# Kernel optimization log

Measured on AMD Instinct MI355X. Metric: run time of the kernel, lower is better.

The kernel has to match this reference:

```python
import jax, jax.numpy as jnp
import numpy as np

N_NODES = 50000
N_EDGES = 800000
N_LABEL_EDGES = 200000
IN_CH = 256
HID = 64
OUT_CH = 64


def gcn_conv(x, W, b, edge_index, n_nodes):
    """PyG GCNConv: symmetric-normalized aggregation with self-loops.
    out[col] = sum_row norm(row,col) * (x @ W)[row] + b
    """
    xw = x @ W  # [N, out]
    loops = jnp.arange(n_nodes, dtype=edge_index.dtype)
    row = jnp.concatenate([edge_index[0], loops])  # source
    col = jnp.concatenate([edge_index[1], loops])  # target
    deg = jax.ops.segment_sum(jnp.ones_like(col, dtype=xw.dtype), col, num_segments=n_nodes)
    dis = jnp.where(deg > 0, jax.lax.rsqrt(deg), 0.0)
    norm = dis[row] * dis[col]  # [E+N]
    out = jax.ops.segment_sum(xw[row] * norm[:, None], col, num_segments=n_nodes)
    return out + b


def setup_inputs() -> dict:
    key = jax.random.key(0)
    k0, k1, k2, k3, k4 = jax.random.split(key, 5)
    x = jax.random.normal(k0, (N_NODES, IN_CH), dtype=jnp.float32)
    edge_index = jax.random.randint(k1, (2, N_EDGES), 0, N_NODES, dtype=jnp.int32)
    edge_label_index = jax.random.randint(k2, (2, N_LABEL_EDGES), 0, N_NODES, dtype=jnp.int32)
    W1 = jax.random.normal(k3, (IN_CH, HID), dtype=jnp.float32) * (1.0 / np.sqrt(IN_CH))
    b1 = jnp.zeros((HID,), dtype=jnp.float32)
    W2 = jax.random.normal(k4, (HID, OUT_CH), dtype=jnp.float32) * (1.0 / np.sqrt(HID))
    b2 = jnp.zeros((OUT_CH,), dtype=jnp.float32)
    return {"x": x, "edge_index": edge_index, "edge_label_index": edge_label_index,
            "W1": W1, "b1": b1, "W2": W2, "b2": b2}


def reference(x, edge_index, edge_label_index, W1, b1, W2, b2):
    n = x.shape[0]
    # encode: two GCNConv layers with ReLU between
    h = jax.nn.relu(gcn_conv(x, W1, b1, edge_index, n))
    z = gcn_conv(h, W2, b2, edge_index, n)
    # decode: gather node pairs, elementwise multiply, sum over features
    src, dst = edge_label_index[0], edge_label_index[1]
    return jnp.sum(z[src] * z[dst], axis=1)  # [N_LABEL_EDGES]
```

## Files before the change

kernel.cpp:

```cpp
#include <hip/hip_runtime.h>
#include <hip/hip_bf16.h>


constexpr int NC = 512;
constexpr int NBPAD = 256;
constexpr int BSHIFT = 8;

using short8 = __attribute__((ext_vector_type(8))) short;
using f32x4 = __attribute__((ext_vector_type(4))) float;

__device__ __forceinline__ unsigned short f2bf(float f) {
    unsigned u = __float_as_uint(f);
    return (unsigned short)((u + 0x7FFF + ((u >> 16) & 1)) >> 16);
}
__device__ __forceinline__ float bf2f(unsigned short h) {
    return __uint_as_float(((unsigned)h) << 16);
}

__global__ __launch_bounds__(256) void pack_kernel(const float* __restrict__ W1,
                                                   const float* __restrict__ W2,
                                                   unsigned short* __restrict__ Wp1,
                                                   unsigned short* __restrict__ Wp2,
                                                   int* __restrict__ bsums) {
    const int t = threadIdx.x, b = blockIdx.x;
    if (b == 0) {
        bsums[t] = 0;
    } else if (b <= 64) {
        const int idx = (b - 1) * 256 + t;
        const int k = idx >> 6, c = idx & 63;
        Wp1[((k >> 3) * 64 + c) * 8 + (k & 7)] = f2bf(W1[idx]);
    } else {
        const int idx = (b - 65) * 256 + t;
        const int k = idx >> 6, c = idx & 63;
        Wp2[((k >> 3) * 64 + c) * 8 + (k & 7)] = f2bf(W2[idx]);
    }
}

__global__ __launch_bounds__(256) void hist_kernel(const int* __restrict__ col,
                                                   int* __restrict__ histBM,
                                                   int* __restrict__ bsums, int E, int CE) {
    __shared__ int hl[NBPAD];
    const int t = threadIdx.x, c = blockIdx.x;
    hl[t] = 0;
    __syncthreads();
    const int s = c * CE, e = min(E, s + CE);
    for (int i = s + t; i < e; i += 256) atomicAdd(&hl[col[i] >> BSHIFT], 1);
    __syncthreads();
    const int v = hl[t];
    histBM[t * NC + c] = v;
    if (v) atomicAdd(&bsums[t], v);
}

__global__ __launch_bounds__(256) void rowscan_kernel(const int* __restrict__ histBM,
                                                      const int* __restrict__ bsums,
                                                      int* __restrict__ offsBM) {
    __shared__ int red[256];
    __shared__ int sc[256];
    const int t = threadIdx.x, b = blockIdx.x;
    red[t] = (t < b) ? bsums[t] : 0;
    __syncthreads();
    for (int off = 128; off > 0; off >>= 1) {
        if (t < off) red[t] += red[t + off];
        __syncthreads();
    }
    const int base = red[0];
    const int2 a = *(const int2*)&histBM[b * NC + 2 * t];
    const int a0 = a.x, a1 = a.y;
    const int ps = a0 + a1;
    sc[t] = ps;
    __syncthreads();
    for (int off = 1; off < 256; off <<= 1) {
        int u = (t >= off) ? sc[t - off] : 0;
        __syncthreads();
        sc[t] += u;
        __syncthreads();
    }
    const int excl = sc[t] - ps;
    offsBM[b * NC + 2 * t] = base + excl;
    offsBM[b * NC + 2 * t + 1] = base + excl + a0;
}

__global__ __launch_bounds__(256) void reorder_kernel(const int* __restrict__ row,
                                                      const int* __restrict__ col,
                                                      const int* __restrict__ offsBM,
                                                      int* __restrict__ part, int E, int CE) {
    __shared__ int cur[NBPAD];
    const int t = threadIdx.x, c = blockIdx.x;
    cur[t] = offsBM[t * NC + c];
    __syncthreads();
    const int s = c * CE, e = min(E, s + CE);
    for (int i = s + t; i < e; i += 256) {
        const int r = row[i], cl = col[i];
        const int p = atomicAdd(&cur[cl >> BSHIFT], 1);
        part[p] = (r << 8) | (cl & 255);
    }
}

__global__ __launch_bounds__(1024) void bucket_csr_kernel(const int* __restrict__ part,
                                                          const int* __restrict__ offsBM,
                                                          int* __restrict__ csr,
                                                          int* __restrict__ offs,
                                                          float* __restrict__ dis,
                                                          int N, int E, int nbk) {
    __shared__ int cnt[256];
    __shared__ int sc[256];
    const int t = threadIdx.x, b = blockIdx.x;
    const int base = b << BSHIFT;
    const int bstart = offsBM[b * NC];
    const int bend = (b + 1 < NBPAD) ? offsBM[(b + 1) * NC] : E;
    const int m = bend - bstart;
    if (t < 256) cnt[t] = 0;
    __syncthreads();
    for (int i = t; i < m; i += 1024) atomicAdd(&cnt[part[bstart + i] & 255], 1);
    __syncthreads();
    int v = 0;
    if (t < 256) { v = cnt[t]; sc[t] = v; }
    __syncthreads();
    for (int off = 1; off < 256; off <<= 1) {
        int u = 0;
        if (t >= off && t < 256) u = sc[t - off];
        __syncthreads();
        if (t < 256) sc[t] += u;
        __syncthreads();
    }
    if (t < 256) {
        const int excl = sc[t] - v;
        const int node = base + t;
        if (node < N) {
            offs[node] = bstart + excl;
            dis[node] = rsqrtf((float)(v + 1));
        }
        sc[t] = excl;
    }
    __syncthreads();
    for (int i = t; i < m; i += 1024) {
        const int pc = part[bstart + i];
        const int p = atomicAdd(&sc[pc & 255], 1);
        csr[bstart + p] = pc >> 8;
    }
    if (b == nbk - 1 && t == 0) offs[N] = E;
}

template <int K>
__global__ __launch_bounds__(256) void gemm_mfma(const float* __restrict__ X,
                                                 const unsigned short* __restrict__ Wp,
                                                 const float* __restrict__ rowscale,
                                                 unsigned short* __restrict__ Y, int nrows) {
    const int tid = threadIdx.x;
    const int wv = tid >> 6;
    const int lane = tid & 63;
    const int m = lane & 15;
    const int quad = lane >> 4;
    const int rowbase = blockIdx.x * 64 + wv * 16;

    int grow = rowbase + m;
    if (grow >= nrows) grow = nrows - 1;
    const float* xrow = X + (long)grow * K + quad * 8;

    f32x4 acc0 = {0.f, 0.f, 0.f, 0.f};
    f32x4 acc1 = acc0, acc2 = acc0, acc3 = acc0;

    #pragma unroll
    for (int ks = 0; ks < K / 32; ++ks) {
        const float4 a0 = *(const float4*)(xrow + ks * 32);
        const float4 a1 = *(const float4*)(xrow + ks * 32 + 4);
        short8 af;
        af[0] = (short)f2bf(a0.x); af[1] = (short)f2bf(a0.y);
        af[2] = (short)f2bf(a0.z); af[3] = (short)f2bf(a0.w);
        af[4] = (short)f2bf(a1.x); af[5] = (short)f2bf(a1.y);
        af[6] = (short)f2bf(a1.z); af[7] = (short)f2bf(a1.w);
        const unsigned short* bp = Wp + (size_t)((ks * 4 + quad) * 64) * 8;
        const short8 b0 = *(const short8*)(bp + (0 * 16 + m) * 8);
        const short8 b1 = *(const short8*)(bp + (1 * 16 + m) * 8);
        const short8 b2 = *(const short8*)(bp + (2 * 16 + m) * 8);
        const short8 b3 = *(const short8*)(bp + (3 * 16 + m) * 8);
        acc0 = __builtin_amdgcn_mfma_f32_16x16x32_bf16(af, b0, acc0, 0, 0, 0);
        acc1 = __builtin_amdgcn_mfma_f32_16x16x32_bf16(af, b1, acc1, 0, 0, 0);
        acc2 = __builtin_amdgcn_mfma_f32_16x16x32_bf16(af, b2, acc2, 0, 0, 0);
        acc3 = __builtin_amdgcn_mfma_f32_16x16x32_bf16(af, b3, acc3, 0, 0, 0);
    }

    #pragma unroll
    for (int reg = 0; reg < 4; ++reg) {
        const int orow = rowbase + quad * 4 + reg;
        if (orow < nrows) {
            const float d = rowscale[orow];
            unsigned short* yp = Y + (size_t)orow * 64 + m;
            yp[0]  = f2bf(d * acc0[reg]);
            yp[16] = f2bf(d * acc1[reg]);
            yp[32] = f2bf(d * acc2[reg]);
            yp[48] = f2bf(d * acc3[reg]);
        }
    }
}

__device__ __forceinline__ void acc8(float* a, short8 v) {
    #pragma unroll
    for (int j = 0; j < 8; ++j) a[j] += bf2f((unsigned short)v[j]);
}

__device__ __forceinline__ void agg_edges(const unsigned short* __restrict__ xs,
                                          const int* __restrict__ csr,
                                          int s, int e, int off, float* acc) {
    int j = s;
    int r0 = 0, r1 = 0, r2 = 0, r3 = 0, r4 = 0, r5 = 0, r6 = 0, r7 = 0;
    if (j + 7 < e) {
        r0 = csr[j];     r1 = csr[j + 1]; r2 = csr[j + 2]; r3 = csr[j + 3];
        r4 = csr[j + 4]; r5 = csr[j + 5]; r6 = csr[j + 6]; r7 = csr[j + 7];
    }
    while (j + 7 < e) {
        const int jn = j + 8;
        const int em1 = e - 1;
        const int n0 = csr[min(jn,     em1)], n1 = csr[min(jn + 1, em1)];
        const int n2 = csr[min(jn + 2, em1)], n3 = csr[min(jn + 3, em1)];
        const int n4 = csr[min(jn + 4, em1)], n5 = csr[min(jn + 5, em1)];
        const int n6 = csr[min(jn + 6, em1)], n7 = csr[min(jn + 7, em1)];
        const short8 v0 = *(const short8*)(xs + (size_t)r0 * 64 + off);
        const short8 v1 = *(const short8*)(xs + (size_t)r1 * 64 + off);
        const short8 v2 = *(const short8*)(xs + (size_t)r2 * 64 + off);
        const short8 v3 = *(const short8*)(xs + (size_t)r3 * 64 + off);
        const short8 v4 = *(const short8*)(xs + (size_t)r4 * 64 + off);
        const short8 v5 = *(const short8*)(xs + (size_t)r5 * 64 + off);
        const short8 v6 = *(const short8*)(xs + (size_t)r6 * 64 + off);
        const short8 v7 = *(const short8*)(xs + (size_t)r7 * 64 + off);
        acc8(acc, v0); acc8(acc, v1); acc8(acc, v2); acc8(acc, v3);
        acc8(acc, v4); acc8(acc, v5); acc8(acc, v6); acc8(acc, v7);
        r0 = n0; r1 = n1; r2 = n2; r3 = n3;
        r4 = n4; r5 = n5; r6 = n6; r7 = n7;
        j = jn;
    }
    for (; j < e; ++j) {
        const int r = csr[j];
        const short8 v = *(const short8*)(xs + (size_t)r * 64 + off);
        acc8(acc, v);
    }
}

__global__ __launch_bounds__(512) void agg_gemm_fused(const unsigned short* __restrict__ xs,
                                                      const int* __restrict__ csr,
                                                      const int* __restrict__ offs,
                                                      const float* __restrict__ dis,
                                                      const float* __restrict__ b1,
                                                      const unsigned short* __restrict__ Wp2,
                                                      unsigned short* __restrict__ Y, int n) {
    __shared__ float lbuf[4 * 4 * 4 * 64];
    const int tid = threadIdx.x;
    const int wp = tid >> 6;
    const int g = wp >> 1;
    const int hf = wp & 1;
    const int lane = tid & 63;
    const int m = lane & 15;
    const int q = lane >> 4;
    const int rowbase = blockIdx.x * 64 + g * 16;

    int i = rowbase + m;
    if (i >= n) i = n - 1;
    const int off = hf * 32 + q * 8;

    float acc[8];
    {
        const short8 s0 = *(const short8*)(xs + (size_t)i * 64 + off);
        #pragma unroll
        for (int j = 0; j < 8; ++j) acc[j] = bf2f((unsigned short)s0[j]);
    }
    agg_edges(xs, csr, offs[i], offs[i + 1], off, acc);

    const float di = dis[i];
    float bl[8];
    *(float4*)&bl[0] = *(const float4*)(b1 + off);
    *(float4*)&bl[4] = *(const float4*)(b1 + off + 4);
    short8 hfrag;
    #pragma unroll
    for (int jj = 0; jj < 8; ++jj)
        hfrag[jj] = (short)f2bf(fmaxf(fmaf(acc[jj], di, bl[jj]), 0.f));

    const unsigned short* bp = Wp2 + (size_t)((hf * 4 + q) * 64) * 8;
    const short8 w0 = *(const short8*)(bp + (0 * 16 + m) * 8);
    const short8 w1 = *(const short8*)(bp + (1 * 16 + m) * 8);
    const short8 w2 = *(const short8*)(bp + (2 * 16 + m) * 8);
    const short8 w3 = *(const short8*)(bp + (3 * 16 + m) * 8);
    f32x4 c0 = {0.f, 0.f, 0.f, 0.f};
    f32x4 c1 = c0, c2 = c0, c3 = c0;
    c0 = __builtin_amdgcn_mfma_f32_16x16x32_bf16(hfrag, w0, c0, 0, 0, 0);
    c1 = __builtin_amdgcn_mfma_f32_16x16x32_bf16(hfrag, w1, c1, 0, 0, 0);
    c2 = __builtin_amdgcn_mfma_f32_16x16x32_bf16(hfrag, w2, c2, 0, 0, 0);
    c3 = __builtin_amdgcn_mfma_f32_16x16x32_bf16(hfrag, w3, c3, 0, 0, 0);

    if (hf == 1) {
        float* lb = lbuf + ((g * 4 + 0) * 4) * 64 + lane;
        #pragma unroll
        for (int reg = 0; reg < 4; ++reg) {
            lb[(0 * 4 + reg) * 64] = c0[reg];
            lb[(1 * 4 + reg) * 64] = c1[reg];
            lb[(2 * 4 + reg) * 64] = c2[reg];
            lb[(3 * 4 + reg) * 64] = c3[reg];
        }
    }
    __syncthreads();
    if (hf == 0) {
        const float* lb = lbuf + ((g * 4 + 0) * 4) * 64 + lane;
        #pragma unroll
        for (int reg = 0; reg < 4; ++reg) {
            const int orow = rowbase + q * 4 + reg;
            if (orow < n) {
                const float d2 = dis[orow];
                unsigned short* yp = Y + (size_t)orow * 64 + m;
                yp[0]  = f2bf(d2 * (c0[reg] + lb[(0 * 4 + reg) * 64]));
                yp[16] = f2bf(d2 * (c1[reg] + lb[(1 * 4 + reg) * 64]));
                yp[32] = f2bf(d2 * (c2[reg] + lb[(2 * 4 + reg) * 64]));
                yp[48] = f2bf(d2 * (c3[reg] + lb[(3 * 4 + reg) * 64]));
            }
        }
    }
}

__global__ __launch_bounds__(256) void agg_wave(const unsigned short* __restrict__ xs,
                                                const int* __restrict__ csr,
                                                const int* __restrict__ offs,
                                                const float* __restrict__ dis,
                                                const float* __restrict__ bias,
                                                unsigned short* __restrict__ Y, int n) {
    const int tid = threadIdx.x;
    const int wv = tid >> 6;
    const int lane = tid & 63;
    const int m = lane & 15;
    const int q = lane >> 4;
    const int hf = blockIdx.y;
    const int rowbase = blockIdx.x * 64 + wv * 16;

    int i = rowbase + m;
    if (i >= n) i = n - 1;
    const int off = hf * 32 + q * 8;

    float acc[8];
    {
        const short8 s0 = *(const short8*)(xs + (size_t)i * 64 + off);
        #pragma unroll
        for (int j = 0; j < 8; ++j) acc[j] = bf2f((unsigned short)s0[j]);
    }
    agg_edges(xs, csr, offs[i], offs[i + 1], off, acc);

    const float di = dis[i];
    float bl[8];
    *(float4*)&bl[0] = *(const float4*)(bias + off);
    *(float4*)&bl[4] = *(const float4*)(bias + off + 4);
    short8 o;
    #pragma unroll
    for (int jj = 0; jj < 8; ++jj)
        o[jj] = (short)f2bf(fmaf(acc[jj], di, bl[jj]));
    *(short8*)(Y + (size_t)i * 64 + off) = o;
}

__global__ __launch_bounds__(256) void decode_kernel(const unsigned short* __restrict__ z,
                                                     const int* __restrict__ src,
                                                     const int* __restrict__ dst,
                                                     float* __restrict__ out, int L) {
    const int t = blockIdx.x * 256 + threadIdx.x;
    const int e = t >> 3;
    const int fl = t & 7;
    if (e >= L) return;
    const int s = src[e];
    const int d = dst[e];
    const short8 a = *(const short8*)&z[(long)s * 64 + fl * 8];
    const short8 b = *(const short8*)&z[(long)d * 64 + fl * 8];
    float p = 0.f;
    #pragma unroll
    for (int j = 0; j < 8; ++j)
        p = fmaf(bf2f((unsigned short)a[j]), bf2f((unsigned short)b[j]), p);
    p += __shfl_xor(p, 4); p += __shfl_xor(p, 2); p += __shfl_xor(p, 1);
    if (fl == 0) out[e] = p;
}

extern "C" void kernel_launch(void* const* d_in, const int* in_sizes, int n_in,
                              void* d_out, int out_size, void* d_ws, size_t ws_size,
                              hipStream_t stream) {
    const float* x   = (const float*)d_in[0];
    const int*   ei  = (const int*)d_in[1];
    const int*   eli = (const int*)d_in[2];
    const float* W1  = (const float*)d_in[3];
    const float* b1  = (const float*)d_in[4];
    const float* W2  = (const float*)d_in[5];
    const float* b2  = (const float*)d_in[6];
    float* out = (float*)d_out;

    const int N = in_sizes[0] / 256;
    const int E = in_sizes[1] / 2;
    const int L = in_sizes[2] / 2;
    const int* row = ei;
    const int* col = ei + E;
    const int* src = eli;
    const int* dst = eli + L;

    char* w = (char*)d_ws;
    unsigned short* xs1 = (unsigned short*)w;  w += (size_t)N * 64 * 2;
    unsigned short* xs2 = (unsigned short*)w;  w += (size_t)N * 64 * 2;
    unsigned short* z = (unsigned short*)w;  w += (size_t)N * 64 * 2;
    int*   csr = (int*)w;    w += (size_t)E * 4;
    int*   offs = (int*)w;   w += (size_t)(N + 1) * 4;
    float* dis = (float*)w;  w += (size_t)N * 4;
    int*   part = (int*)w;   w += (size_t)E * 4;
    int* histBM = (int*)w;   w += (size_t)NBPAD * NC * 4;
    int* offsBM = (int*)w;   w += (size_t)NBPAD * NC * 4;
    int* bsums  = (int*)w;   w += NBPAD * 4;
    unsigned short* Wp1 = (unsigned short*)w;  w += (size_t)256 * 64 * 2;
    unsigned short* Wp2 = (unsigned short*)w;  w += (size_t)64 * 64 * 2;

    const int CE = (E + NC - 1) / NC;
    const int nbk = (N + (1 << BSHIFT) - 1) >> BSHIFT;

    pack_kernel<<<81, 256, 0, stream>>>(W1, W2, Wp1, Wp2, bsums);
    hist_kernel<<<NC, 256, 0, stream>>>(col, histBM, bsums, E, CE);
    rowscan_kernel<<<NBPAD, 256, 0, stream>>>(histBM, bsums, offsBM);
    reorder_kernel<<<NC, 256, 0, stream>>>(row, col, offsBM, part, E, CE);
    bucket_csr_kernel<<<nbk, 1024, 0, stream>>>(part, offsBM, csr, offs, dis, N, E, nbk);

    gemm_mfma<256><<<(N + 63) / 64, 256, 0, stream>>>(x, Wp1, dis, xs1, N);
    agg_gemm_fused<<<(N + 63) / 64, 512, 0, stream>>>(xs1, csr, offs, dis, b1, Wp2, xs2, N);
    agg_wave<<<dim3((N + 63) / 64, 2), 256, 0, stream>>>(xs2, csr, offs, dis, b2, z, N);
    decode_kernel<<<(L * 8 + 255) / 256, 256, 0, stream>>>(z, src, dst, out, L);
}
```

Baseline: 213.6 us.

## Split feature matrices into column halves for cache-resident gather passes

Stores every 64-wide bf16 node feature matrix as two separate 32-column halves. Each aggregation and decode stage then runs as two passes, and each pass gathers from a 3.2MB array that is more likely to stay in L2/LLC. The fused aggregate+GEMM kernel is split into two aggregation passes plus a standalone second GEMM, and CSR reads use nontemporal loads. In exchange it adds kernel launches, reads the CSR structure twice per layer, and does a read-modify-write on the output in the second decode pass.

```diff
diff --git a/kernel.cpp b/kernel.cpp
--- a/kernel.cpp
+++ b/kernel.cpp
@@ -145,7 +145,8 @@
 __global__ __launch_bounds__(256) void gemm_mfma(const float* __restrict__ X,
                                                  const unsigned short* __restrict__ Wp,
                                                  const float* __restrict__ rowscale,
-                                                 unsigned short* __restrict__ Y, int nrows) {
+                                                 unsigned short* __restrict__ Ylo,
+                                                 unsigned short* __restrict__ Yhi, int nrows) {
     const int tid = threadIdx.x;
     const int wv = tid >> 6;
     const int lane = tid & 63;
@@ -185,11 +186,10 @@
         const int orow = rowbase + quad * 4 + reg;
         if (orow < nrows) {
             const float d = rowscale[orow];
-            unsigned short* yp = Y + (size_t)orow * 64 + m;
-            yp[0]  = f2bf(d * acc0[reg]);
-            yp[16] = f2bf(d * acc1[reg]);
-            yp[32] = f2bf(d * acc2[reg]);
-            yp[48] = f2bf(d * acc3[reg]);
+            Ylo[(size_t)orow * 32 + m]      = f2bf(d * acc0[reg]);
+            Ylo[(size_t)orow * 32 + 16 + m] = f2bf(d * acc1[reg]);
+            Yhi[(size_t)orow * 32 + m]      = f2bf(d * acc2[reg]);
+            Yhi[(size_t)orow * 32 + 16 + m] = f2bf(d * acc3[reg]);
         }
     }
 }
@@ -199,30 +199,64 @@
     for (int j = 0; j < 8; ++j) a[j] += bf2f((unsigned short)v[j]);
 }
 
-__device__ __forceinline__ void agg_edges(const unsigned short* __restrict__ xs,
-                                          const int* __restrict__ csr,
-                                          int s, int e, int off, float* acc) {
+template <bool RELU>
+__global__ __launch_bounds__(256) void agg_half(const unsigned short* __restrict__ xsh,
+                                                const int* __restrict__ csr,
+                                                const int* __restrict__ offs,
+                                                const float* __restrict__ dis,
+                                                const float* __restrict__ biash,
+                                                unsigned short* __restrict__ outh, int n) {
+    const int tid = threadIdx.x;
+    const int wv = tid >> 6;
+    const int lane = tid & 63;
+    const int m = lane & 15;
+    const int q = lane >> 4;
+    const int rowbase = blockIdx.x * 64 + wv * 16;
+
+    int i = rowbase + m;
+    if (i >= n) i = n - 1;
+    const int off = q * 8;
+
+    float acc[8];
+    {
+        const short8 s0 = *(const short8*)(xsh + (size_t)i * 32 + off);
+        #pragma unroll
+        for (int j = 0; j < 8; ++j) acc[j] = bf2f((unsigned short)s0[j]);
+    }
+
+    const int s = offs[i];
+    const int e = offs[i + 1];
     int j = s;
     int r0 = 0, r1 = 0, r2 = 0, r3 = 0, r4 = 0, r5 = 0, r6 = 0, r7 = 0;
     if (j + 7 < e) {
-        r0 = csr[j];     r1 = csr[j + 1]; r2 = csr[j + 2]; r3 = csr[j + 3];
-        r4 = csr[j + 4]; r5 = csr[j + 5]; r6 = csr[j + 6]; r7 = csr[j + 7];
+        r0 = __builtin_nontemporal_load(csr + j);
+        r1 = __builtin_nontemporal_load(csr + j + 1);
+        r2 = __builtin_nontemporal_load(csr + j + 2);
+        r3 = __builtin_nontemporal_load(csr + j + 3);
+        r4 = __builtin_nontemporal_load(csr + j + 4);
+        r5 = __builtin_nontemporal_load(csr + j + 5);
+        r6 = __builtin_nontemporal_load(csr + j + 6);
+        r7 = __builtin_nontemporal_load(csr + j + 7);
     }
     while (j + 7 < e) {
         const int jn = j + 8;
         const int em1 = e - 1;
-        const int n0 = csr[min(jn,     em1)], n1 = csr[min(jn + 1, em1)];
-        const int n2 = csr[min(jn + 2, em1)], n3 = csr[min(jn + 3, em1)];
-        const int n4 = csr[min(jn + 4, em1)], n5 = csr[min(jn + 5, em1)];
-        const int n6 = csr[min(jn + 6, em1)], n7 = csr[min(jn + 7, em1)];
-        const short8 v0 = *(const short8*)(xs + (size_t)r0 * 64 + off);
-        const short8 v1 = *(const short8*)(xs + (size_t)r1 * 64 + off);
-        const short8 v2 = *(const short8*)(xs + (size_t)r2 * 64 + off);
-        const short8 v3 = *(const short8*)(xs + (size_t)r3 * 64 + off);
-        const short8 v4 = *(const short8*)(xs + (size_t)r4 * 64 + off);
-        const short8 v5 = *(const short8*)(xs + (size_t)r5 * 64 + off);
-        const short8 v6 = *(const short8*)(xs + (size_t)r6 * 64 + off);
-        const short8 v7 = *(const short8*)(xs + (size_t)r7 * 64 + off);
+        const int n0 = __builtin_nontemporal_load(csr + min(jn,     em1));
+        const int n1 = __builtin_nontemporal_load(csr + min(jn + 1, em1));
+        const int n2 = __builtin_nontemporal_load(csr + min(jn + 2, em1));
+        const int n3 = __builtin_nontemporal_load(csr + min(jn + 3, em1));
+        const int n4 = __builtin_nontemporal_load(csr + min(jn + 4, em1));
+        const int n5 = __builtin_nontemporal_load(csr + min(jn + 5, em1));
+        const int n6 = __builtin_nontemporal_load(csr + min(jn + 6, em1));
+        const int n7 = __builtin_nontemporal_load(csr + min(jn + 7, em1));
+        const short8 v0 = *(const short8*)(xsh + (size_t)r0 * 32 + off);
+        const short8 v1 = *(const short8*)(xsh + (size_t)r1 * 32 + off);
+        const short8 v2 = *(const short8*)(xsh + (size_t)r2 * 32 + off);
+        const short8 v3 = *(const short8*)(xsh + (size_t)r3 * 32 + off);
+        const short8 v4 = *(const short8*)(xsh + (size_t)r4 * 32 + off);
+        const short8 v5 = *(const short8*)(xsh + (size_t)r5 * 32 + off);
+        const short8 v6 = *(const short8*)(xsh + (size_t)r6 * 32 + off);
+        const short8 v7 = *(const short8*)(xsh + (size_t)r7 * 32 + off);
         acc8(acc, v0); acc8(acc, v1); acc8(acc, v2); acc8(acc, v3);
         acc8(acc, v4); acc8(acc, v5); acc8(acc, v6); acc8(acc, v7);
         r0 = n0; r1 = n1; r2 = n2; r3 = n3;
@@ -230,145 +264,98 @@
         j = jn;
     }
     for (; j < e; ++j) {
-        const int r = csr[j];
-        const short8 v = *(const short8*)(xs + (size_t)r * 64 + off);
+        const int r = __builtin_nontemporal_load(csr + j);
+        const short8 v = *(const short8*)(xsh + (size_t)r * 32 + off);
         acc8(acc, v);
     }
-}
-
-__global__ __launch_bounds__(512) void agg_gemm_fused(const unsigned short* __restrict__ xs,
-                                                      const int* __restrict__ csr,
-                                                      const int* __restrict__ offs,
-                                                      const float* __restrict__ dis,
-                                                      const float* __restrict__ b1,
-                                                      const unsigned short* __restrict__ Wp2,
-                                                      unsigned short* __restrict__ Y, int n) {
-    __shared__ float lbuf[4 * 4 * 4 * 64];
-    const int tid = threadIdx.x;
-    const int wp = tid >> 6;
-    const int g = wp >> 1;
-    const int hf = wp & 1;
-    const int lane = tid & 63;
-    const int m = lane & 15;
-    const int q = lane >> 4;
-    const int rowbase = blockIdx.x * 64 + g * 16;
-
-    int i = rowbase + m;
-    if (i >= n) i = n - 1;
-    const int off = hf * 32 + q * 8;
-
-    float acc[8];
-    {
-        const short8 s0 = *(const short8*)(xs + (size_t)i * 64 + off);
-        #pragma unroll
-        for (int j = 0; j < 8; ++j) acc[j] = bf2f((unsigned short)s0[j]);
-    }
-    agg_edges(xs, csr, offs[i], offs[i + 1], off, acc);
 
     const float di = dis[i];
     float bl[8];
-    *(float4*)&bl[0] = *(const float4*)(b1 + off);
-    *(float4*)&bl[4] = *(const float4*)(b1 + off + 4);
-    short8 hfrag;
-    #pragma unroll
-    for (int jj = 0; jj < 8; ++jj)
-        hfrag[jj] = (short)f2bf(fmaxf(fmaf(acc[jj], di, bl[jj]), 0.f));
-
-    const unsigned short* bp = Wp2 + (size_t)((hf * 4 + q) * 64) * 8;
-    const short8 w0 = *(const short8*)(bp + (0 * 16 + m) * 8);
-    const short8 w1 = *(const short8*)(bp + (1 * 16 + m) * 8);
-    const short8 w2 = *(const short8*)(bp + (2 * 16 + m) * 8);
-    const short8 w3 = *(const short8*)(bp + (3 * 16 + m) * 8);
-    f32x4 c0 = {0.f, 0.f, 0.f, 0.f};
-    f32x4 c1 = c0, c2 = c0, c3 = c0;
-    c0 = __builtin_amdgcn_mfma_f32_16x16x32_bf16(hfrag, w0, c0, 0, 0, 0);
-    c1 = __builtin_amdgcn_mfma_f32_16x16x32_bf16(hfrag, w1, c1, 0, 0, 0);
-    c2 = __builtin_amdgcn_mfma_f32_16x16x32_bf16(hfrag, w2, c2, 0, 0, 0);
-    c3 = __builtin_amdgcn_mfma_f32_16x16x32_bf16(hfrag, w3, c3, 0, 0, 0);
-
-    if (hf == 1) {
-        float* lb = lbuf + ((g * 4 + 0) * 4) * 64 + lane;
-        #pragma unroll
-        for (int reg = 0; reg < 4; ++reg) {
-            lb[(0 * 4 + reg) * 64] = c0[reg];
-            lb[(1 * 4 + reg) * 64] = c1[reg];
-            lb[(2 * 4 + reg) * 64] = c2[reg];
-            lb[(3 * 4 + reg) * 64] = c3[reg];
-        }
-    }
-    __syncthreads();
-    if (hf == 0) {
-        const float* lb = lbuf + ((g * 4 + 0) * 4) * 64 + lane;
-        #pragma unroll
-        for (int reg = 0; reg < 4; ++reg) {
-            const int orow = rowbase + q * 4 + reg;
-            if (orow < n) {
-                const float d2 = dis[orow];
-                unsigned short* yp = Y + (size_t)orow * 64 + m;
-                yp[0]  = f2bf(d2 * (c0[reg] + lb[(0 * 4 + reg) * 64]));
-                yp[16] = f2bf(d2 * (c1[reg] + lb[(1 * 4 + reg) * 64]));
-                yp[32] = f2bf(d2 * (c2[reg] + lb[(2 * 4 + reg) * 64]));
-                yp[48] = f2bf(d2 * (c3[reg] + lb[(3 * 4 + reg) * 64]));
-            }
-        }
-    }
-}
-
-__global__ __launch_bounds__(256) void agg_wave(const unsigned short* __restrict__ xs,
-                                                const int* __restrict__ csr,
-                                                const int* __restrict__ offs,
-                                                const float* __restrict__ dis,
-                                                const float* __restrict__ bias,
-                                                unsigned short* __restrict__ Y, int n) {
+    *(float4*)&bl[0] = *(const float4*)(biash + off);
+    *(float4*)&bl[4] = *(const float4*)(biash + off + 4);
+    short8 o;
+    #pragma unroll
+    for (int jj = 0; jj < 8; ++jj) {
+        const float v = fmaf(acc[jj], di, bl[jj]);
+        o[jj] = (short)f2bf(RELU ? fmaxf(v, 0.f) : v);
+    }
+    *(short8*)(outh + (size_t)i * 32 + off) = o;
+}
+
+__global__ __launch_bounds__(256) void gemm2_mfma(const unsigned short* __restrict__ hL,
+                                                  const unsigned short* __restrict__ hH,
+                                                  const unsigned short* __restrict__ Wp2,
+                                                  const float* __restrict__ dis,
+                                                  unsigned short* __restrict__ Ylo,
+                                                  unsigned short* __restrict__ Yhi, int n) {
     const int tid = threadIdx.x;
     const int wv = tid >> 6;
     const int lane = tid & 63;
     const int m = lane & 15;
     const int q = lane >> 4;
-    const int hf = blockIdx.y;
     const int rowbase = blockIdx.x * 64 + wv * 16;
 
-    int i = rowbase + m;
-    if (i >= n) i = n - 1;
-    const int off = hf * 32 + q * 8;
-
-    float acc[8];
-    {
-        const short8 s0 = *(const short8*)(xs + (size_t)i * 64 + off);
-        #pragma unroll
-        for (int j = 0; j < 8; ++j) acc[j] = bf2f((unsigned short)s0[j]);
-    }
-    agg_edges(xs, csr, offs[i], offs[i + 1], off, acc);
-
-    const float di = dis[i];
-    float bl[8];
-    *(float4*)&bl[0] = *(const float4*)(bias + off);
-    *(float4*)&bl[4] = *(const float4*)(bias + off + 4);
-    short8 o;
-    #pragma unroll
-    for (int jj = 0; jj < 8; ++jj)
-        o[jj] = (short)f2bf(fmaf(acc[jj], di, bl[jj]));
-    *(short8*)(Y + (size_t)i * 64 + off) = o;
-}
-
-__global__ __launch_bounds__(256) void decode_kernel(const unsigned short* __restrict__ z,
-                                                     const int* __restrict__ src,
-                                                     const int* __restrict__ dst,
-                                                     float* __restrict__ out, int L) {
+    int grow = rowbase + m;
+    if (grow >= n) grow = n - 1;
+    const short8 ha = *(const short8*)(hL + (size_t)grow * 32 + q * 8);
+    const short8 hb = *(const short8*)(hH + (size_t)grow * 32 + q * 8);
+
+    const unsigned short* bplo = Wp2 + (size_t)(q * 64) * 8;
+    const unsigned short* bphi = Wp2 + (size_t)((4 + q) * 64) * 8;
+    const short8 w0l = *(const short8*)(bplo + (0 * 16 + m) * 8);
+    const short8 w1l = *(const short8*)(bplo + (1 * 16 + m) * 8);
+    const short8 w2l = *(const short8*)(bplo + (2 * 16 + m) * 8);
+    const short8 w3l = *(const short8*)(bplo + (3 * 16 + m) * 8);
+    const short8 w0h = *(const short8*)(bphi + (0 * 16 + m) * 8);
+    const short8 w1h = *(const short8*)(bphi + (1 * 16 + m) * 8);
+    const short8 w2h = *(const short8*)(bphi + (2 * 16 + m) * 8);
+    const short8 w3h = *(const short8*)(bphi + (3 * 16 + m) * 8);
+    f32x4 c0 = {0.f, 0.f, 0.f, 0.f};
+    f32x4 c1 = c0, c2 = c0, c3 = c0;
+    c0 = __builtin_amdgcn_mfma_f32_16x16x32_bf16(ha, w0l, c0, 0, 0, 0);
+    c0 = __builtin_amdgcn_mfma_f32_16x16x32_bf16(hb, w0h, c0, 0, 0, 0);
+    c1 = __builtin_amdgcn_mfma_f32_16x16x32_bf16(ha, w1l, c1, 0, 0, 0);
+    c1 = __builtin_amdgcn_mfma_f32_16x16x32_bf16(hb, w1h, c1, 0, 0, 0);
+    c2 = __builtin_amdgcn_mfma_f32_16x16x32_bf16(ha, w2l, c2, 0, 0, 0);
+    c2 = __builtin_amdgcn_mfma_f32_16x16x32_bf16(hb, w2h, c2, 0, 0, 0);
+    c3 = __builtin_amdgcn_mfma_f32_16x16x32_bf16(ha, w3l, c3, 0, 0, 0);
+    c3 = __builtin_amdgcn_mfma_f32_16x16x32_bf16(hb, w3h, c3, 0, 0, 0);
+
+    #pragma unroll
+    for (int reg = 0; reg < 4; ++reg) {
+        const int orow = rowbase + q * 4 + reg;
+        if (orow < n) {
+            const float d2 = dis[orow];
+            Ylo[(size_t)orow * 32 + m]      = f2bf(d2 * c0[reg]);
+            Ylo[(size_t)orow * 32 + 16 + m] = f2bf(d2 * c1[reg]);
+            Yhi[(size_t)orow * 32 + m]      = f2bf(d2 * c2[reg]);
+            Yhi[(size_t)orow * 32 + 16 + m] = f2bf(d2 * c3[reg]);
+        }
+    }
+}
+
+template <bool FIRST>
+__global__ __launch_bounds__(256) void decode_half(const unsigned short* __restrict__ zh,
+                                                   const int* __restrict__ src,
+                                                   const int* __restrict__ dst,
+                                                   float* __restrict__ out, int L) {
     const int t = blockIdx.x * 256 + threadIdx.x;
-    const int e = t >> 3;
-    const int fl = t & 7;
+    const int e = t >> 2;
+    const int fl = t & 3;
     if (e >= L) return;
     const int s = src[e];
     const int d = dst[e];
-    const short8 a = *(const short8*)&z[(long)s * 64 + fl * 8];
-    const short8 b = *(const short8*)&z[(long)d * 64 + fl * 8];
+    const short8 a = *(const short8*)&zh[(size_t)s * 32 + fl * 8];
+    const short8 b = *(const short8*)&zh[(size_t)d * 32 + fl * 8];
     float p = 0.f;
     #pragma unroll
     for (int j = 0; j < 8; ++j)
         p = fmaf(bf2f((unsigned short)a[j]), bf2f((unsigned short)b[j]), p);
-    p += __shfl_xor(p, 4); p += __shfl_xor(p, 2); p += __shfl_xor(p, 1);
-    if (fl == 0) out[e] = p;
+    p += __shfl_xor(p, 2); p += __shfl_xor(p, 1);
+    if (fl == 0) {
+        if (FIRST) out[e] = p;
+        else out[e] += p;
+    }
 }
 
 extern "C" void kernel_launch(void* const* d_in, const int* in_sizes, int n_in,
@@ -392,9 +379,14 @@
     const int* dst = eli + L;
 
     char* w = (char*)d_ws;
-    unsigned short* xs1 = (unsigned short*)w;  w += (size_t)N * 64 * 2;
-    unsigned short* xs2 = (unsigned short*)w;  w += (size_t)N * 64 * 2;
-    unsigned short* z = (unsigned short*)w;  w += (size_t)N * 64 * 2;
+    unsigned short* xs1_lo = (unsigned short*)w;  w += (size_t)N * 32 * 2;
+    unsigned short* xs1_hi = (unsigned short*)w;  w += (size_t)N * 32 * 2;
+    unsigned short* hL     = (unsigned short*)w;  w += (size_t)N * 32 * 2;
+    unsigned short* hH     = (unsigned short*)w;  w += (size_t)N * 32 * 2;
+    unsigned short* xs2_lo = (unsigned short*)w;  w += (size_t)N * 32 * 2;
+    unsigned short* xs2_hi = (unsigned short*)w;  w += (size_t)N * 32 * 2;
+    unsigned short* z_lo   = (unsigned short*)w;  w += (size_t)N * 32 * 2;
+    unsigned short* z_hi   = (unsigned short*)w;  w += (size_t)N * 32 * 2;
     int*   csr = (int*)w;    w += (size_t)E * 4;
     int*   offs = (int*)w;   w += (size_t)(N + 1) * 4;
     float* dis = (float*)w;  w += (size_t)N * 4;
@@ -407,6 +399,7 @@
 
     const int CE = (E + NC - 1) / NC;
     const int nbk = (N + (1 << BSHIFT) - 1) >> BSHIFT;
+    const int NB64 = (N + 63) / 64;
 
     pack_kernel<<<81, 256, 0, stream>>>(W1, W2, Wp1, Wp2, bsums);
     hist_kernel<<<NC, 256, 0, stream>>>(col, histBM, bsums, E, CE);
@@ -414,8 +407,12 @@
     reorder_kernel<<<NC, 256, 0, stream>>>(row, col, offsBM, part, E, CE);
     bucket_csr_kernel<<<nbk, 1024, 0, stream>>>(part, offsBM, csr, offs, dis, N, E, nbk);
 
-    gemm_mfma<256><<<(N + 63) / 64, 256, 0, stream>>>(x, Wp1, dis, xs1, N);
-    agg_gemm_fused<<<(N + 63) / 64, 512, 0, stream>>>(xs1, csr, offs, dis, b1, Wp2, xs2, N);
-    agg_wave<<<dim3((N + 63) / 64, 2), 256, 0, stream>>>(xs2, csr, offs, dis, b2, z, N);
-    decode_kernel<<<(L * 8 + 255) / 256, 256, 0, stream>>>(z, src, dst, out, L);
-}
+    gemm_mfma<256><<<NB64, 256, 0, stream>>>(x, Wp1, dis, xs1_lo, xs1_hi, N);
+    agg_half<true><<<NB64, 256, 0, stream>>>(xs1_lo, csr, offs, dis, b1,      hL, N);
+    agg_half<true><<<NB64, 256, 0, stream>>>(xs1_hi, csr, offs, dis, b1 + 32, hH, N);
+    gemm2_mfma<<<NB64, 256, 0, stream>>>(hL, hH, Wp2, dis, xs2_lo, xs2_hi, N);
+    agg_half<false><<<NB64, 256, 0, stream>>>(xs2_lo, csr, offs, dis, b2,      z_lo, N);
+    agg_half<false><<<NB64, 256, 0, stream>>>(xs2_hi, csr, offs, dis, b2 + 32, z_hi, N);
+    decode_half<true><<<(L * 4 + 255) / 256, 256, 0, stream>>>(z_lo, src, dst, out, L);
+    decode_half<false><<<(L * 4 + 255) / 256, 256, 0, stream>>>(z_hi, src, dst, out, L);
+}
```

Measured after the change: 233.8 us. +9.4%, slower.
